# Kernel optimization log

Measured on AMD Instinct MI355X. Metric: run time of the kernel, lower is better.

## Reference

```python
import jax, jax.numpy as jnp
import numpy as np

B, C, C1, C2, H, W = 16, 64, 16, 64, 128, 128

def setup_inputs() -> dict:
    key = jax.random.key(0)
    ks = jax.random.split(key, 8)
    s1 = 1.0 / np.sqrt(C1)
    s2 = 1.0 / np.sqrt(C)
    return {
        "x": jax.random.normal(ks[0], (B, C, H, W), dtype=jnp.float32),
        "e": jax.random.normal(ks[1], (B, C1, H, W), dtype=jnp.float32),
        "W1": jax.random.uniform(ks[2], (C2, C1), jnp.float32, -s1, s1),
        "b1": jax.random.uniform(ks[3], (C2,), jnp.float32, -s1, s1),
        "W2": jax.random.uniform(ks[4], (C2, C), jnp.float32, -s2, s2),
        "b2": jax.random.uniform(ks[5], (C2,), jnp.float32, -s2, s2),
        "W3": jax.random.uniform(ks[6], (C2, C), jnp.float32, -s2, s2),
        "b3": jax.random.uniform(ks[7], (C2,), jnp.float32, -s2, s2),
    }

def _conv1x1(inp, Wm, bv):
    # (B,Cin,H,W) x (Cout,Cin) -> (B,Cout,H,W)
    return jnp.einsum('bchw,oc->bohw', inp, Wm) + bv[None, :, None, None]

def reference(x, e, W1, b1, W2, b2, W3, b3):
    Bn, _, Hn, Wn = x.shape
    Q = _conv1x1(e, W1, b1).reshape(-1, Hn, Wn)   # (B*C2, H, W)
    V = _conv1x1(x, W2, b2).reshape(-1, Hn, Wn)
    K = _conv1x1(x, W3, b3).reshape(-1, Hn, Wn)
    score = jnp.einsum('nhw,ngw->nhg', Q, V)      # (B*C2, H, H), no scaling
    attn = jax.nn.softmax(score, axis=-1)
    ctx = jnp.einsum('nhg,ngw->nhw', attn, K)     # (B*C2, H, W)
    return ctx.reshape(Bn, -1, Hn, Wn)
```

## Files before the change

### kernel.cpp

```cpp
#include <hip/hip_runtime.h>

typedef __bf16 bf16_t;
typedef __bf16 bf16x8 __attribute__((ext_vector_type(8)));
typedef float f32x4 __attribute__((ext_vector_type(4)));
typedef unsigned short u16x4_t __attribute__((ext_vector_type(4)));

#define HW 16384
#define LOG2E 1.44269504088896f

__device__ __forceinline__ bf16_t f2b(float f) {
  unsigned u = __builtin_bit_cast(unsigned, f);
  u += 0x7fff + ((u >> 16) & 1);
  unsigned short s = (unsigned short)(u >> 16);
  return __builtin_bit_cast(bf16_t, s);
}
__device__ __forceinline__ unsigned short b2u(bf16_t b) {
  return __builtin_bit_cast(unsigned short, b);
}

__global__ __launch_bounds__(256, 3) void qvk_kernel(
    const float* __restrict__ x, const float* __restrict__ e,
    const float* __restrict__ W1, const float* __restrict__ b1,
    const float* __restrict__ W2, const float* __restrict__ b2,
    const float* __restrict__ W3, const float* __restrict__ b3,
    bf16_t* __restrict__ Qg, bf16_t* __restrict__ Vg, bf16_t* __restrict__ Kg)
{
  __shared__ bf16_t lx[256 * 64];
  __shared__ bf16_t le[256 * 32];

  const int t = threadIdx.x;
  const int lane = t & 63;
  const int wv = t >> 6;
  const int b = blockIdx.x >> 6;
  const int p0 = (blockIdx.x & 63) << 8;

  {
    const int cq = wv << 3;
#pragma unroll
    for (int half = 0; half < 2; ++half) {
      const int cc = cq + half * 32;
#pragma unroll
      for (int pp = 0; pp < 4; ++pp) {
        const int pl = pp * 64 + lane;
        const float* src = x + (size_t)(b * 64 + cc) * HW + p0 + pl;
        bf16x8 v;
#pragma unroll
        for (int i = 0; i < 8; ++i) v[i] = f2b(src[(size_t)i * HW]);
        int byte = pl * 128 + cc * 2;
        byte ^= (pl & 7) << 4;
        *reinterpret_cast<bf16x8*>(reinterpret_cast<char*>(lx) + byte) = v;
      }
    }
  }
  {
    const int cq = (t & 3) << 3;
    const int pb = t >> 2;
#pragma unroll
    for (int pp = 0; pp < 4; ++pp) {
      const int pl = pp * 64 + pb;
      bf16x8 v;
#pragma unroll
      for (int i = 0; i < 8; ++i) {
        const int c = cq + i;
        float f = (c < 16) ? e[(size_t)(b * 16 + c) * HW + p0 + pl] : 0.0f;
        v[i] = f2b(f);
      }
      *reinterpret_cast<bf16x8*>(reinterpret_cast<char*>(le) + pl * 64 + cq * 2) = v;
    }
  }
  __syncthreads();

  const int pw0 = wv << 6;
  const int lr = lane & 15;
  const int lg = lane >> 4;
  const int kq = lg << 3;

  auto ldx = [&](int row, int c) -> bf16x8 {
    int byte = row * 128 + c * 2;
    byte ^= (row & 7) << 4;
    return *reinterpret_cast<const bf16x8*>(reinterpret_cast<const char*>(lx) + byte);
  };

  f32x4 acc[4][4];

  auto do_xtarget = [&](const float* __restrict__ Wm, const float* __restrict__ bias,
                        bf16_t* __restrict__ G) {
#pragma unroll
    for (int mt = 0; mt < 4; ++mt)
#pragma unroll
      for (int nt = 0; nt < 4; ++nt) acc[mt][nt] = f32x4{0.f, 0.f, 0.f, 0.f};
#pragma unroll
    for (int kt = 0; kt < 2; ++kt) {
      bf16x8 Bw[4], Af[4];
#pragma unroll
      for (int nt = 0; nt < 4; ++nt) {
        const float* wp = Wm + (size_t)(nt * 16 + lr) * 64 + kt * 32 + kq;
        bf16x8 a;
#pragma unroll
        for (int i = 0; i < 8; ++i) a[i] = f2b(wp[i]);
        Bw[nt] = a;
      }
#pragma unroll
      for (int mt = 0; mt < 4; ++mt) Af[mt] = ldx(pw0 + mt * 16 + lr, kt * 32 + kq);
#pragma unroll
      for (int mt = 0; mt < 4; ++mt)
#pragma unroll
        for (int nt = 0; nt < 4; ++nt)
          acc[mt][nt] = __builtin_amdgcn_mfma_f32_16x16x32_bf16(Af[mt], Bw[nt], acc[mt][nt], 0, 0, 0);
    }
    float bvv[4];
#pragma unroll
    for (int nt = 0; nt < 4; ++nt) bvv[nt] = bias[nt * 16 + lr];
#pragma unroll
    for (int nt = 0; nt < 4; ++nt)
#pragma unroll
      for (int mt = 0; mt < 4; ++mt) {
        u16x4_t pk;
#pragma unroll
        for (int r = 0; r < 4; ++r) pk[r] = b2u(f2b(acc[mt][nt][r] + bvv[nt]));
        *reinterpret_cast<u16x4_t*>(G + (size_t)(b * 64 + nt * 16 + lr) * HW
                                      + p0 + pw0 + mt * 16 + (lg << 2)) = pk;
      }
  };

  do_xtarget(W2, b2, Vg);
  do_xtarget(W3, b3, Kg);

#pragma unroll
  for (int mt = 0; mt < 4; ++mt)
#pragma unroll
    for (int nt = 0; nt < 4; ++nt) acc[mt][nt] = f32x4{0.f, 0.f, 0.f, 0.f};
  {
    bf16x8 Bw[4], Af[4];
#pragma unroll
    for (int nt = 0; nt < 4; ++nt) {
      bf16x8 a;
      if (kq < 16) {
        const float* wp = W1 + (size_t)(nt * 16 + lr) * 16 + kq;
#pragma unroll
        for (int i = 0; i < 8; ++i) a[i] = f2b(wp[i]);
      } else {
#pragma unroll
        for (int i = 0; i < 8; ++i) a[i] = f2b(0.0f);
      }
      Bw[nt] = a;
    }
#pragma unroll
    for (int mt = 0; mt < 4; ++mt)
      Af[mt] = *reinterpret_cast<const bf16x8*>(
          reinterpret_cast<const char*>(le) + (pw0 + mt * 16 + lr) * 64 + kq * 2);
#pragma unroll
    for (int mt = 0; mt < 4; ++mt)
#pragma unroll
      for (int nt = 0; nt < 4; ++nt)
        acc[mt][nt] = __builtin_amdgcn_mfma_f32_16x16x32_bf16(Af[mt], Bw[nt], acc[mt][nt], 0, 0, 0);
  }
  {
    float bvv[4];
#pragma unroll
    for (int nt = 0; nt < 4; ++nt) bvv[nt] = b1[nt * 16 + lr];
#pragma unroll
    for (int nt = 0; nt < 4; ++nt)
#pragma unroll
      for (int mt = 0; mt < 4; ++mt) {
        u16x4_t pk;
#pragma unroll
        for (int r = 0; r < 4; ++r) pk[r] = b2u(f2b(acc[mt][nt][r] + bvv[nt]));
        *reinterpret_cast<u16x4_t*>(Qg + (size_t)(b * 64 + nt * 16 + lr) * HW
                                      + p0 + pw0 + mt * 16 + (lg << 2)) = pk;
      }
  }
}

__global__ __launch_bounds__(256, 2) void attn_kernel(
    const bf16_t* __restrict__ Qg, const bf16_t* __restrict__ Vg,
    const bf16_t* __restrict__ Kg, float* __restrict__ out)
{
  __shared__ bf16_t bufK[128 * 128];
  __shared__ bf16_t bufV[128 * 128];
  __shared__ float zl[128];

  const int n = blockIdx.x;
  const int t = threadIdx.x;
  const int lane = t & 63;
  const int wv = t >> 6;
  const int lr = lane & 15;
  const int lg = lane >> 4;
  const int kq = lg << 3;
  const int h0 = wv << 5;

  const bf16_t* Qn = Qg + (size_t)n * HW;
  const bf16_t* Vn = Vg + (size_t)n * HW;
  const bf16_t* Kn = Kg + (size_t)n * HW;

  bf16x8 qf[4][2];
#pragma unroll
  for (int kt = 0; kt < 4; ++kt)
#pragma unroll
    for (int mt = 0; mt < 2; ++mt)
      qf[kt][mt] = *reinterpret_cast<const bf16x8*>(
          Qn + (h0 + mt * 16 + lr) * 128 + kt * 32 + kq);

#pragma unroll
  for (int it = 0; it < 8; ++it) {
    const int chunk = it * 256 + t;
    const int row = chunk >> 4;
    int byte = (row << 8) + ((chunk & 15) << 4);
    byte ^= (row & 7) << 4;
    *reinterpret_cast<bf16x8*>(reinterpret_cast<char*>(bufV) + byte) =
        *reinterpret_cast<const bf16x8*>(Vn + chunk * 8);
  }
#pragma unroll
  for (int it = 0; it < 8; ++it) {
    const int w = t & 127;
    const int g0 = ((it << 1) + (t >> 7)) << 3;
    bf16x8 v;
#pragma unroll
    for (int i = 0; i < 8; ++i) v[i] = Kn[(g0 + i) * 128 + w];
    int byte = (w << 8) + (g0 << 1);
    byte ^= (w & 7) << 4;
    *reinterpret_cast<bf16x8*>(reinterpret_cast<char*>(bufK) + byte) = v;
  }
  __syncthreads();

  auto ldfrag = [&](const bf16_t* buf, int row, int c) -> bf16x8 {
    int byte = (row << 8) + (c << 1);
    byte ^= (row & 7) << 4;
    return *reinterpret_cast<const bf16x8*>(reinterpret_cast<const char*>(buf) + byte);
  };

  f32x4 acc[2][8];
#pragma unroll
  for (int mt = 0; mt < 2; ++mt)
#pragma unroll
    for (int nt = 0; nt < 8; ++nt) acc[mt][nt] = f32x4{0.f, 0.f, 0.f, 0.f};
#pragma unroll
  for (int kt = 0; kt < 4; ++kt) {
#pragma unroll
    for (int nt = 0; nt < 8; ++nt) {
      bf16x8 Bv = ldfrag(bufV, nt * 16 + lr, kt * 32 + kq);
      acc[0][nt] = __builtin_amdgcn_mfma_f32_16x16x32_bf16(qf[kt][0], Bv, acc[0][nt], 0, 0, 0);
      acc[1][nt] = __builtin_amdgcn_mfma_f32_16x16x32_bf16(qf[kt][1], Bv, acc[1][nt], 0, 0, 0);
    }
  }

  float zrow[2][4];
#pragma unroll
  for (int mt = 0; mt < 2; ++mt) {
#pragma unroll
    for (int r = 0; r < 4; ++r) {
      float m = acc[mt][0][r];
#pragma unroll
      for (int nt = 1; nt < 8; ++nt) m = fmaxf(m, acc[mt][nt][r]);
      m = fmaxf(m, __shfl_xor(m, 1));
      m = fmaxf(m, __shfl_xor(m, 2));
      m = fmaxf(m, __shfl_xor(m, 4));
      m = fmaxf(m, __shfl_xor(m, 8));
      float z = 0.f;
#pragma unroll
      for (int nt = 0; nt < 8; ++nt) {
        float p = exp2f((acc[mt][nt][r] - m) * LOG2E);
        acc[mt][nt][r] = p;
        z += p;
      }
      z += __shfl_xor(z, 1);
      z += __shfl_xor(z, 2);
      z += __shfl_xor(z, 4);
      z += __shfl_xor(z, 8);
      zrow[mt][r] = z;
    }
  }
  __syncthreads();

#pragma unroll
  for (int mt = 0; mt < 2; ++mt) {
    const int rbase = h0 + mt * 16 + (lg << 2);
    if (lr == 0) {
#pragma unroll
      for (int r = 0; r < 4; ++r) zl[rbase + r] = 1.0f / zrow[mt][r];
    }
#pragma unroll
    for (int nt = 0; nt < 8; ++nt) {
#pragma unroll
      for (int r = 0; r < 4; ++r) {
        const int row = rbase + r;
        int byte = (row << 8) + ((nt * 16 + lr) << 1);
        byte ^= (row & 7) << 4;
        *reinterpret_cast<bf16_t*>(reinterpret_cast<char*>(bufV) + byte) = f2b(acc[mt][nt][r]);
      }
    }
  }
  __syncthreads();

  f32x4 acc2[2][8];
#pragma unroll
  for (int mt = 0; mt < 2; ++mt)
#pragma unroll
    for (int nt = 0; nt < 8; ++nt) acc2[mt][nt] = f32x4{0.f, 0.f, 0.f, 0.f};
#pragma unroll
  for (int kt = 0; kt < 4; ++kt) {
    bf16x8 A0 = ldfrag(bufK, h0 + lr,      kt * 32 + kq);
    bf16x8 A1 = ldfrag(bufK, h0 + 16 + lr, kt * 32 + kq);
#pragma unroll
    for (int nt = 0; nt < 8; ++nt) {
      bf16x8 Bp = ldfrag(bufV, nt * 16 + lr, kt * 32 + kq);
      acc2[0][nt] = __builtin_amdgcn_mfma_f32_16x16x32_bf16(A0, Bp, acc2[0][nt], 0, 0, 0);
      acc2[1][nt] = __builtin_amdgcn_mfma_f32_16x16x32_bf16(A1, Bp, acc2[1][nt], 0, 0, 0);
    }
  }

  float* On = out + (size_t)n * HW;
#pragma unroll
  for (int nt = 0; nt < 8; ++nt) {
    const float zv = zl[nt * 16 + lr];
#pragma unroll
    for (int mt = 0; mt < 2; ++mt) {
      f32x4 o;
#pragma unroll
      for (int r = 0; r < 4; ++r) o[r] = acc2[mt][nt][r] * zv;
      *reinterpret_cast<f32x4*>(On + (size_t)(nt * 16 + lr) * 128
                                + h0 + mt * 16 + (lg << 2)) = o;
    }
  }
}

extern "C" void kernel_launch(void* const* d_in, const int* in_sizes, int n_in,
                              void* d_out, int out_size, void* d_ws, size_t ws_size,
                              hipStream_t stream) {
  const float* x  = (const float*)d_in[0];
  const float* e  = (const float*)d_in[1];
  const float* W1 = (const float*)d_in[2];
  const float* b1 = (const float*)d_in[3];
  const float* W2 = (const float*)d_in[4];
  const float* b2 = (const float*)d_in[5];
  const float* W3 = (const float*)d_in[6];
  const float* b3 = (const float*)d_in[7];
  float* out = (float*)d_out;

  bf16_t* Qg = (bf16_t*)d_ws;
  bf16_t* Vg = Qg + (size_t)1024 * HW;
  bf16_t* Kg = Vg + (size_t)1024 * HW;

  qvk_kernel<<<1024, 256, 0, stream>>>(x, e, W1, b1, W2, b2, W3, b3, Qg, Vg, Kg);
  attn_kernel<<<1024, 256, 0, stream>>>(Qg, Vg, Kg, out);
}
```

Before: 215.9 us.

## Vectorize projection loads, stage weights in LDS, and defer K transpose in attention

The projection kernel now handles 128 pixels per block with twice as many blocks. It loads x and e with float4 vector loads instead of scalar strided reads, and converts the weights to bf16 once into shared memory instead of reloading them per fragment from global. In the attention kernel, K is fetched with coalesced row-vector loads into registers and transposed into LDS only after the QV MFMA loop, so those loads can overlap with compute. A new XOR swizzle is applied to all LDS layouts. The cost is higher register pressure from holding V and K in registers, plus scalar LDS stores for the K transpose.

After: 196.2 us. -9.1%, faster.

```diff
diff --git a/kernel.cpp b/kernel.cpp
--- a/kernel.cpp
+++ b/kernel.cpp
@@ -17,6 +17,8 @@
 __device__ __forceinline__ unsigned short b2u(bf16_t b) {
   return __builtin_bit_cast(unsigned short, b);
 }
+__device__ __forceinline__ int swz8(int row) { return ((row ^ (row >> 3)) & 7) << 4; }
+__device__ __forceinline__ int swz4v(int row) { return (row ^ (row >> 2)) & 3; }
 
 __global__ __launch_bounds__(256, 3) void qvk_kernel(
     const float* __restrict__ x, const float* __restrict__ e,
@@ -25,96 +27,166 @@
     const float* __restrict__ W3, const float* __restrict__ b3,
     bf16_t* __restrict__ Qg, bf16_t* __restrict__ Vg, bf16_t* __restrict__ Kg)
 {
-  __shared__ bf16_t lx[256 * 64];
-  __shared__ bf16_t le[256 * 32];
+  __shared__ bf16_t lx[128 * 64];
+  __shared__ bf16_t le[128 * 32];
+  __shared__ bf16_t w2b[64 * 64];
+  __shared__ bf16_t w3b[64 * 64];
+  __shared__ bf16_t w1b[64 * 32];
 
   const int t = threadIdx.x;
   const int lane = t & 63;
   const int wv = t >> 6;
-  const int b = blockIdx.x >> 6;
-  const int p0 = (blockIdx.x & 63) << 8;
-
-  {
-    const int cq = wv << 3;
-#pragma unroll
-    for (int half = 0; half < 2; ++half) {
-      const int cc = cq + half * 32;
-#pragma unroll
-      for (int pp = 0; pp < 4; ++pp) {
-        const int pl = pp * 64 + lane;
-        const float* src = x + (size_t)(b * 64 + cc) * HW + p0 + pl;
-        bf16x8 v;
-#pragma unroll
-        for (int i = 0; i < 8; ++i) v[i] = f2b(src[(size_t)i * HW]);
-        int byte = pl * 128 + cc * 2;
-        byte ^= (pl & 7) << 4;
-        *reinterpret_cast<bf16x8*>(reinterpret_cast<char*>(lx) + byte) = v;
-      }
-    }
-  }
-  {
-    const int cq = (t & 3) << 3;
-    const int pb = t >> 2;
-#pragma unroll
-    for (int pp = 0; pp < 4; ++pp) {
-      const int pl = pp * 64 + pb;
-      bf16x8 v;
-#pragma unroll
-      for (int i = 0; i < 8; ++i) {
-        const int c = cq + i;
-        float f = (c < 16) ? e[(size_t)(b * 16 + c) * HW + p0 + pl] : 0.0f;
-        v[i] = f2b(f);
-      }
-      *reinterpret_cast<bf16x8*>(reinterpret_cast<char*>(le) + pl * 64 + cq * 2) = v;
-    }
-  }
-  __syncthreads();
-
-  const int pw0 = wv << 6;
+  const int b = blockIdx.x >> 7;
+  const int p0 = (blockIdx.x & 127) << 7;
   const int lr = lane & 15;
   const int lg = lane >> 4;
   const int kq = lg << 3;
 
-  auto ldx = [&](int row, int c) -> bf16x8 {
-    int byte = row * 128 + c * 2;
-    byte ^= (row & 7) << 4;
-    return *reinterpret_cast<const bf16x8*>(reinterpret_cast<const char*>(lx) + byte);
+  const int li = lane & 31;
+  const int h2 = lane >> 5;
+  const int cbase = wv * 16 + h2 * 8;
+  f32x4 xr[8];
+#pragma unroll
+  for (int j = 0; j < 8; ++j)
+    xr[j] = *reinterpret_cast<const f32x4*>(
+        x + (size_t)(b * 64 + cbase + j) * HW + p0 + li * 4);
+
+  const int ec = t >> 4;
+  const int ep = (t & 15) * 4;
+  f32x4 er[2];
+#pragma unroll
+  for (int j = 0; j < 2; ++j)
+    er[j] = *reinterpret_cast<const f32x4*>(
+        e + (size_t)(b * 16 + ec) * HW + p0 + ep + j * 64);
+
+  const int wo = t >> 2;
+  const int wc = (t & 3) * 16;
+  f32x4 w2r[4], w3r[4];
+#pragma unroll
+  for (int k = 0; k < 4; ++k) {
+    w2r[k] = *reinterpret_cast<const f32x4*>(W2 + (size_t)wo * 64 + wc + k * 4);
+    w3r[k] = *reinterpret_cast<const f32x4*>(W3 + (size_t)wo * 64 + wc + k * 4);
+  }
+  const int w1c = (t & 3) * 4;
+  f32x4 w1r = *reinterpret_cast<const f32x4*>(W1 + (size_t)wo * 16 + w1c);
+
+  float bv1[4], bv2[4], bv3[4];
+#pragma unroll
+  for (int nt = 0; nt < 4; ++nt) {
+    bv1[nt] = b1[nt * 16 + lr];
+    bv2[nt] = b2[nt * 16 + lr];
+    bv3[nt] = b3[nt * 16 + lr];
+  }
+
+  {
+    const int chunk = cbase >> 3;
+#pragma unroll
+    for (int r = 0; r < 4; ++r) {
+      const int row = li * 4 + r;
+      bf16x8 v;
+#pragma unroll
+      for (int j = 0; j < 8; ++j) v[j] = f2b(xr[j][r]);
+      *reinterpret_cast<bf16x8*>(reinterpret_cast<char*>(lx)
+          + row * 128 + ((chunk << 4) ^ swz8(row))) = v;
+    }
+  }
+#pragma unroll
+  for (int j = 0; j < 2; ++j)
+#pragma unroll
+    for (int r = 0; r < 4; ++r) {
+      const int row = ep + j * 64 + r;
+      const int byte = row * 64 + ((((ec >> 3) ^ swz4v(row)) << 4)) + (ec & 7) * 2;
+      *reinterpret_cast<bf16_t*>(reinterpret_cast<char*>(le) + byte) = f2b(er[j][r]);
+    }
+  {
+    const int row = t >> 1;
+    const int chunk = 2 + (t & 1);
+    bf16x8 zv;
+#pragma unroll
+    for (int k = 0; k < 8; ++k) zv[k] = f2b(0.0f);
+    *reinterpret_cast<bf16x8*>(reinterpret_cast<char*>(le)
+        + row * 64 + ((chunk ^ swz4v(row)) << 4)) = zv;
+  }
+  {
+    const int ch0 = (t & 3) * 2;
+    bf16x8 a, c2;
+#pragma unroll
+    for (int k = 0; k < 8; ++k) {
+      a[k]  = f2b(w2r[k >> 2][k & 3]);
+      c2[k] = f2b(w2r[2 + (k >> 2)][k & 3]);
+    }
+    *reinterpret_cast<bf16x8*>(reinterpret_cast<char*>(w2b)
+        + wo * 128 + ((ch0 << 4) ^ swz8(wo))) = a;
+    *reinterpret_cast<bf16x8*>(reinterpret_cast<char*>(w2b)
+        + wo * 128 + (((ch0 + 1) << 4) ^ swz8(wo))) = c2;
+#pragma unroll
+    for (int k = 0; k < 8; ++k) {
+      a[k]  = f2b(w3r[k >> 2][k & 3]);
+      c2[k] = f2b(w3r[2 + (k >> 2)][k & 3]);
+    }
+    *reinterpret_cast<bf16x8*>(reinterpret_cast<char*>(w3b)
+        + wo * 128 + ((ch0 << 4) ^ swz8(wo))) = a;
+    *reinterpret_cast<bf16x8*>(reinterpret_cast<char*>(w3b)
+        + wo * 128 + (((ch0 + 1) << 4) ^ swz8(wo))) = c2;
+  }
+  {
+    typedef __bf16 bf16x4_ __attribute__((ext_vector_type(4)));
+    bf16x4_ a;
+#pragma unroll
+    for (int k = 0; k < 4; ++k) a[k] = f2b(w1r[k]);
+    const int byte = wo * 64 + (((w1c >> 3) ^ swz4v(wo)) << 4) + (w1c & 4) * 2;
+    *reinterpret_cast<bf16x4_*>(reinterpret_cast<char*>(w1b) + byte) = a;
+    if (t < 128) {
+      const int row = t >> 1;
+      const int chunk = 2 + (t & 1);
+      bf16x8 zv;
+#pragma unroll
+      for (int k = 0; k < 8; ++k) zv[k] = f2b(0.0f);
+      *reinterpret_cast<bf16x8*>(reinterpret_cast<char*>(w1b)
+          + row * 64 + ((chunk ^ swz4v(row)) << 4)) = zv;
+    }
+  }
+  __syncthreads();
+
+  const int pw0 = wv << 5;
+
+  auto ldx = [&](int row, int ce) -> bf16x8 {
+    return *reinterpret_cast<const bf16x8*>(reinterpret_cast<const char*>(lx)
+        + row * 128 + (((ce >> 3) << 4) ^ swz8(row)));
   };
-
-  f32x4 acc[4][4];
-
-  auto do_xtarget = [&](const float* __restrict__ Wm, const float* __restrict__ bias,
-                        bf16_t* __restrict__ G) {
-#pragma unroll
-    for (int mt = 0; mt < 4; ++mt)
+  auto ldw = [&](const bf16_t* wb, int row, int ce) -> bf16x8 {
+    return *reinterpret_cast<const bf16x8*>(reinterpret_cast<const char*>(wb)
+        + row * 128 + (((ce >> 3) << 4) ^ swz8(row)));
+  };
+  auto ld64 = [&](const bf16_t* buf, int row, int ce) -> bf16x8 {
+    return *reinterpret_cast<const bf16x8*>(reinterpret_cast<const char*>(buf)
+        + row * 64 + (((ce >> 3) ^ swz4v(row)) << 4));
+  };
+
+  f32x4 acc[2][4];
+
+  auto do_xtarget = [&](const bf16_t* wb, const float* bvv, bf16_t* __restrict__ G) {
+#pragma unroll
+    for (int mt = 0; mt < 2; ++mt)
 #pragma unroll
       for (int nt = 0; nt < 4; ++nt) acc[mt][nt] = f32x4{0.f, 0.f, 0.f, 0.f};
 #pragma unroll
     for (int kt = 0; kt < 2; ++kt) {
-      bf16x8 Bw[4], Af[4];
-#pragma unroll
-      for (int nt = 0; nt < 4; ++nt) {
-        const float* wp = Wm + (size_t)(nt * 16 + lr) * 64 + kt * 32 + kq;
-        bf16x8 a;
-#pragma unroll
-        for (int i = 0; i < 8; ++i) a[i] = f2b(wp[i]);
-        Bw[nt] = a;
-      }
-#pragma unroll
-      for (int mt = 0; mt < 4; ++mt) Af[mt] = ldx(pw0 + mt * 16 + lr, kt * 32 + kq);
-#pragma unroll
-      for (int mt = 0; mt < 4; ++mt)
+      bf16x8 Af[2], Bw[4];
+#pragma unroll
+      for (int mt = 0; mt < 2; ++mt) Af[mt] = ldx(pw0 + mt * 16 + lr, kt * 32 + kq);
+#pragma unroll
+      for (int nt = 0; nt < 4; ++nt) Bw[nt] = ldw(wb, nt * 16 + lr, kt * 32 + kq);
+#pragma unroll
+      for (int mt = 0; mt < 2; ++mt)
 #pragma unroll
         for (int nt = 0; nt < 4; ++nt)
           acc[mt][nt] = __builtin_amdgcn_mfma_f32_16x16x32_bf16(Af[mt], Bw[nt], acc[mt][nt], 0, 0, 0);
     }
-    float bvv[4];
-#pragma unroll
-    for (int nt = 0; nt < 4; ++nt) bvv[nt] = bias[nt * 16 + lr];
 #pragma unroll
     for (int nt = 0; nt < 4; ++nt)
 #pragma unroll
-      for (int mt = 0; mt < 4; ++mt) {
+      for (int mt = 0; mt < 2; ++mt) {
         u16x4_t pk;
 #pragma unroll
         for (int r = 0; r < 4; ++r) pk[r] = b2u(f2b(acc[mt][nt][r] + bvv[nt]));
@@ -123,53 +195,35 @@
       }
   };
 
-  do_xtarget(W2, b2, Vg);
-  do_xtarget(W3, b3, Kg);
-
-#pragma unroll
-  for (int mt = 0; mt < 4; ++mt)
+  do_xtarget(w2b, bv2, Vg);
+  do_xtarget(w3b, bv3, Kg);
+
+#pragma unroll
+  for (int mt = 0; mt < 2; ++mt)
 #pragma unroll
     for (int nt = 0; nt < 4; ++nt) acc[mt][nt] = f32x4{0.f, 0.f, 0.f, 0.f};
   {
-    bf16x8 Bw[4], Af[4];
-#pragma unroll
-    for (int nt = 0; nt < 4; ++nt) {
-      bf16x8 a;
-      if (kq < 16) {
-        const float* wp = W1 + (size_t)(nt * 16 + lr) * 16 + kq;
-#pragma unroll
-        for (int i = 0; i < 8; ++i) a[i] = f2b(wp[i]);
-      } else {
-#pragma unroll
-        for (int i = 0; i < 8; ++i) a[i] = f2b(0.0f);
-      }
-      Bw[nt] = a;
-    }
-#pragma unroll
-    for (int mt = 0; mt < 4; ++mt)
-      Af[mt] = *reinterpret_cast<const bf16x8*>(
-          reinterpret_cast<const char*>(le) + (pw0 + mt * 16 + lr) * 64 + kq * 2);
-#pragma unroll
-    for (int mt = 0; mt < 4; ++mt)
+    bf16x8 Af[2], Bw[4];
+#pragma unroll
+    for (int mt = 0; mt < 2; ++mt) Af[mt] = ld64(le, pw0 + mt * 16 + lr, kq);
+#pragma unroll
+    for (int nt = 0; nt < 4; ++nt) Bw[nt] = ld64(w1b, nt * 16 + lr, kq);
+#pragma unroll
+    for (int mt = 0; mt < 2; ++mt)
 #pragma unroll
       for (int nt = 0; nt < 4; ++nt)
         acc[mt][nt] = __builtin_amdgcn_mfma_f32_16x16x32_bf16(Af[mt], Bw[nt], acc[mt][nt], 0, 0, 0);
   }
-  {
-    float bvv[4];
-#pragma unroll
-    for (int nt = 0; nt < 4; ++nt) bvv[nt] = b1[nt * 16 + lr];
-#pragma unroll
-    for (int nt = 0; nt < 4; ++nt)
-#pragma unroll
-      for (int mt = 0; mt < 4; ++mt) {
-        u16x4_t pk;
-#pragma unroll
-        for (int r = 0; r < 4; ++r) pk[r] = b2u(f2b(acc[mt][nt][r] + bvv[nt]));
-        *reinterpret_cast<u16x4_t*>(Qg + (size_t)(b * 64 + nt * 16 + lr) * HW
-                                      + p0 + pw0 + mt * 16 + (lg << 2)) = pk;
-      }
-  }
+#pragma unroll
+  for (int nt = 0; nt < 4; ++nt)
+#pragma unroll
+    for (int mt = 0; mt < 2; ++mt) {
+      u16x4_t pk;
+#pragma unroll
+      for (int r = 0; r < 4; ++r) pk[r] = b2u(f2b(acc[mt][nt][r] + bv1[nt]));
+      *reinterpret_cast<u16x4_t*>(Qg + (size_t)(b * 64 + nt * 16 + lr) * HW
+                                    + p0 + pw0 + mt * 16 + (lg << 2)) = pk;
+    }
 }
 
 __global__ __launch_bounds__(256, 2) void attn_kernel(
@@ -193,6 +247,18 @@
   const bf16_t* Vn = Vg + (size_t)n * HW;
   const bf16_t* Kn = Kg + (size_t)n * HW;
 
+  bf16x8 vreg[8];
+#pragma unroll
+  for (int it = 0; it < 8; ++it)
+    vreg[it] = *reinterpret_cast<const bf16x8*>(Vn + (it * 256 + t) * 8);
+
+  const int wchunk = t & 15;
+  const int grow = t >> 4;
+  bf16x8 kreg[8];
+#pragma unroll
+  for (int it = 0; it < 8; ++it)
+    kreg[it] = *reinterpret_cast<const bf16x8*>(Kn + (grow + 16 * it) * 128 + wchunk * 8);
+
   bf16x8 qf[4][2];
 #pragma unroll
   for (int kt = 0; kt < 4; ++kt)
@@ -205,28 +271,14 @@
   for (int it = 0; it < 8; ++it) {
     const int chunk = it * 256 + t;
     const int row = chunk >> 4;
-    int byte = (row << 8) + ((chunk & 15) << 4);
-    byte ^= (row & 7) << 4;
-    *reinterpret_cast<bf16x8*>(reinterpret_cast<char*>(bufV) + byte) =
-        *reinterpret_cast<const bf16x8*>(Vn + chunk * 8);
-  }
-#pragma unroll
-  for (int it = 0; it < 8; ++it) {
-    const int w = t & 127;
-    const int g0 = ((it << 1) + (t >> 7)) << 3;
-    bf16x8 v;
-#pragma unroll
-    for (int i = 0; i < 8; ++i) v[i] = Kn[(g0 + i) * 128 + w];
-    int byte = (w << 8) + (g0 << 1);
-    byte ^= (w & 7) << 4;
-    *reinterpret_cast<bf16x8*>(reinterpret_cast<char*>(bufK) + byte) = v;
+    *reinterpret_cast<bf16x8*>(reinterpret_cast<char*>(bufV)
+        + row * 256 + (((chunk & 15) << 4) ^ swz8(row))) = vreg[it];
   }
   __syncthreads();
 
   auto ldfrag = [&](const bf16_t* buf, int row, int c) -> bf16x8 {
-    int byte = (row << 8) + (c << 1);
-    byte ^= (row & 7) << 4;
-    return *reinterpret_cast<const bf16x8*>(reinterpret_cast<const char*>(buf) + byte);
+    return *reinterpret_cast<const bf16x8*>(reinterpret_cast<const char*>(buf)
+        + row * 256 + (((c << 1)) ^ swz8(row)));
   };
 
   f32x4 acc[2][8];
@@ -241,6 +293,17 @@
       bf16x8 Bv = ldfrag(bufV, nt * 16 + lr, kt * 32 + kq);
       acc[0][nt] = __builtin_amdgcn_mfma_f32_16x16x32_bf16(qf[kt][0], Bv, acc[0][nt], 0, 0, 0);
       acc[1][nt] = __builtin_amdgcn_mfma_f32_16x16x32_bf16(qf[kt][1], Bv, acc[1][nt], 0, 0, 0);
+    }
+  }
+
+#pragma unroll
+  for (int it = 0; it < 8; ++it) {
+    const int g = grow + 16 * it;
+#pragma unroll
+    for (int j = 0; j < 8; ++j) {
+      const int w = wchunk * 8 + j;
+      *reinterpret_cast<bf16_t*>(reinterpret_cast<char*>(bufK)
+          + w * 256 + ((g << 1) ^ swz8(w))) = kreg[it][j];
     }
   }
 
@@ -284,9 +347,8 @@
 #pragma unroll
       for (int r = 0; r < 4; ++r) {
         const int row = rbase + r;
-        int byte = (row << 8) + ((nt * 16 + lr) << 1);
-        byte ^= (row & 7) << 4;
-        *reinterpret_cast<bf16_t*>(reinterpret_cast<char*>(bufV) + byte) = f2b(acc[mt][nt][r]);
+        *reinterpret_cast<bf16_t*>(reinterpret_cast<char*>(bufV)
+            + row * 256 + (((nt * 16 + lr) << 1) ^ swz8(row))) = f2b(acc[mt][nt][r]);
       }
     }
   }
@@ -341,6 +403,6 @@
   bf16_t* Vg = Qg + (size_t)1024 * HW;
   bf16_t* Kg = Vg + (size_t)1024 * HW;
 
-  qvk_kernel<<<1024, 256, 0, stream>>>(x, e, W1, b1, W2, b2, W3, b3, Qg, Vg, Kg);
+  qvk_kernel<<<2048, 256, 0, stream>>>(x, e, W1, b1, W2, b2, W3, b3, Qg, Vg, Kg);
   attn_kernel<<<1024, 256, 0, stream>>>(Qg, Vg, Kg, out);
 }
```
